# Kernel optimization log

Hardware: AMD Instinct MI355X
Metric: run time of the kernel (lower is better)

## Reference

```python
import jax, jax.numpy as jnp
import numpy as np

SCALES = [2, 4, 8, 16]
UNIT = np.array([0.015, 0.015, 0.015], dtype=np.float32)
VNUM = np.array([64, 64, 64], dtype=np.float32)
OFFSET = (-0.5 * UNIT * VNUM).astype(np.float32)  # -0.48 per axis

N = 8192
MS = [16000, 4000, 512, 64]
CS = [32, 64, 128, 256]


def setup_inputs() -> dict:
    key = jax.random.key(0)
    ks = jax.random.split(key, 1 + 2 * 4)
    extent = (UNIT * VNUM).astype(np.float32)  # 0.96 per axis
    points = (jax.random.uniform(ks[0], (N, 3), dtype=jnp.float32) - 0.5) * extent
    inp = {"points": points, "batch_ids": jnp.zeros((N,), dtype=jnp.int32)}
    for i, (m, c, s) in enumerate(zip(MS, CS, SCALES)):
        grid = 64 // s
        idx = jax.random.randint(ks[1 + 2 * i], (m, 4), 0, grid, dtype=jnp.int32)
        idx = idx.at[:, 0].set(0)  # single batch
        inp[f"indices{i + 1}"] = idx
        inp[f"feats{i + 1}"] = jax.random.normal(ks[2 + 2 * i], (m, c), dtype=jnp.float32)
    return inp


def _three_nn_interpolate(t_xyz, q_xyz, q_feats):
    # t_xyz: [N,3] targets, q_xyz: [M,3] voxel centers, q_feats: [M,C]
    d2 = jnp.sum((t_xyz[:, None, :] - q_xyz[None, :, :]) ** 2, axis=-1)  # [N,M] squared dists
    neg_d, idx = jax.lax.top_k(-d2, 3)  # 3 nearest neighbors
    dist = -neg_d  # squared distances, as returned by pointnet2 three_nn
    dist_recip = 1.0 / (dist + 1e-8)
    weight = dist_recip / jnp.sum(dist_recip, axis=-1, keepdims=True)  # [N,3]
    return jnp.einsum('nk,nkc->nc', weight, q_feats[idx])  # gather + weighted sum


def reference(points, batch_ids, feats1, indices1, feats2, indices2,
              feats3, indices3, feats4, indices4):
    # batch_ids are all zero (single batch); the CUDA kernel restricts the
    # neighbor search to matching batch, so an xyz-only distance is faithful.
    feat_lists = [feats1, feats2, feats3, feats4]
    idx_lists = [indices1, indices2, indices3, indices4]
    outs = []
    for i, s in enumerate(SCALES):
        voxel_extent = (UNIT * s).astype(np.float32)
        # tensor2points: voxel index -> metric center coordinate
        q_xyz = idx_lists[i][:, 1:].astype(jnp.float32) * voxel_extent + OFFSET + 0.5 * voxel_extent
        outs.append(_three_nn_interpolate(points, q_xyz, feat_lists[i]))
    return jnp.concatenate(outs, axis=1)  # [N, 32+64+128+256]
```

## Files before the change

kernel.cpp:

```cpp
#include <hip/hip_runtime.h>

#define INF_F 3.402823466e+38f

struct Params {
  const float* points;
  const int* idx[4];
  const float* feats[4];
  float2* hdr;
  int* counts;
  int2* cellHdr;
  int* fillcur;
  int* mfill;
  int* cellList;
  int* perm;
  int* cursor;
  float* outp;
  int N, totM, totC;
  int M[4], C[4], Mbase[4], colOff[4], G[4], cellBase[4];
  int cellsTot, lenCounts, allocBlocks;
  float ve[4], hv[4], inv_ve[4];
  float off;
};

__device__ __forceinline__ int spread3(int v) {
  return (v & 1) | ((v & 2) << 2) | ((v & 4) << 4) | ((v & 8) << 6);
}
__device__ __forceinline__ int point_bucket(const float* pts, int i) {
  float x = pts[i * 3 + 0], y = pts[i * 3 + 1], z = pts[i * 3 + 2];
  float sc = 16.0f / 0.96f;
  int cx = (int)((x + 0.48f) * sc);
  int cy = (int)((y + 0.48f) * sc);
  int cz = (int)((z + 0.48f) * sc);
  cx = cx < 0 ? 0 : (cx > 15 ? 15 : cx);
  cy = cy < 0 ? 0 : (cy > 15 ? 15 : cy);
  cz = cz < 0 ? 0 : (cz > 15 ? 15 : cz);
  return spread3(cx) | (spread3(cy) << 1) | (spread3(cz) << 2);
}

__device__ __forceinline__ bool lexlt(float da, int ia, float db, int ib) {
  return da < db || (da == db && ia < ib);
}

__global__ __launch_bounds__(256) void zero_kernel(Params pr) {
  int t = blockIdx.x * 256 + threadIdx.x;
  if (t < pr.lenCounts) pr.counts[t] = 0;
  if (t == 0) pr.cursor[0] = 0;
}

__global__ __launch_bounds__(256) void count_kernel(Params pr) {
  int t = blockIdx.x * 256 + threadIdx.x;
  if (t < pr.totM) {
    int s = (t >= pr.Mbase[1]) + (t >= pr.Mbase[2]) + (t >= pr.Mbase[3]);
    int m = t - pr.Mbase[s];
    const int* id = pr.idx[s] + (size_t)m * 4;
    int G = pr.G[s];
    int cell = (id[1] * G + id[2]) * G + id[3];
    atomicAdd(&pr.counts[pr.cellBase[s] + cell], 1);
  } else if (t < pr.totM + pr.N) {
    int i = t - pr.totM;
    atomicAdd(&pr.counts[pr.cellsTot + point_bucket(pr.points, i)], 1);
  }
}

__global__ __launch_bounds__(256) void alloc_kernel(Params pr) {
  int tid = threadIdx.x;
  int lane = tid & 63, wv = tid >> 6;
  if ((int)blockIdx.x < pr.allocBlocks) {
    int c = blockIdx.x * 256 + tid;
    int cnt = (c < pr.cellsTot) ? pr.counts[c] : 0;
    int inc = cnt;
    for (int off = 1; off < 64; off <<= 1) {
      int u = __shfl_up(inc, off);
      if (lane >= off) inc += u;
    }
    int wtotal = __shfl(inc, 63);
    int basev = 0;
    if (lane == 63 && wtotal > 0) basev = atomicAdd(pr.cursor, wtotal);
    basev = __shfl(basev, 63);
    if (c < pr.cellsTot) {
      int st = basev + inc - cnt;
      pr.cellHdr[c] = make_int2(st, cnt);
      pr.fillcur[c] = st;
    }
    return;
  }
  __shared__ int wt[4];
  const int base = pr.cellsTot;
  int v[16]; int sum = 0;
#pragma unroll
  for (int k = 0; k < 16; ++k) { v[k] = pr.counts[base + tid * 16 + k]; sum += v[k]; }
  int inc = sum;
  for (int off = 1; off < 64; off <<= 1) {
    int u = __shfl_up(inc, off);
    if (lane >= off) inc += u;
  }
  if (lane == 63) wt[wv] = inc;
  __syncthreads();
  int wbase = 0;
  for (int w = 0; w < 4; ++w) wbase += (w < wv) ? wt[w] : 0;
  int run = wbase + inc - sum;
#pragma unroll
  for (int k = 0; k < 16; ++k) { pr.mfill[tid * 16 + k] = run; run += v[k]; }
}

__global__ __launch_bounds__(256) void fill_kernel(Params pr) {
  int t = blockIdx.x * 256 + threadIdx.x;
  if (t < pr.totM) {
    int s = (t >= pr.Mbase[1]) + (t >= pr.Mbase[2]) + (t >= pr.Mbase[3]);
    int m = t - pr.Mbase[s];
    const int* id = pr.idx[s] + (size_t)m * 4;
    int G = pr.G[s];
    int cell = (id[1] * G + id[2]) * G + id[3];
    int pos = atomicAdd(&pr.fillcur[pr.cellBase[s] + cell], 1);
    pr.cellList[pos] = m;
  } else if (t < pr.totM + pr.N) {
    int i = t - pr.totM;
    int pos = atomicAdd(&pr.mfill[point_bucket(pr.points, i)], 1);
    pr.perm[pos] = i;
  }
}

__global__ __launch_bounds__(256) void search_kernel(Params pr) {
#pragma clang fp contract(off)
  int wave = blockIdx.x * 4 + (threadIdx.x >> 6);
  if (wave >= 4 * pr.N) return;
  int lane = threadIdx.x & 63;
  int s = wave / pr.N;
  int slot = wave - s * pr.N;
  int pid = pr.perm[slot];
  float px = pr.points[pid * 3 + 0];
  float py = pr.points[pid * 3 + 1];
  float pz = pr.points[pid * 3 + 2];
  int G = pr.G[s];
  float ve = pr.ve[s], hv = pr.hv[s], off = pr.off, inv = pr.inv_ve[s];
  int cx = (int)((px - off) * inv); cx = cx < 0 ? 0 : (cx > G - 1 ? G - 1 : cx);
  int cy = (int)((py - off) * inv); cy = cy < 0 ? 0 : (cy > G - 1 ? G - 1 : cy);
  int cz = (int)((pz - off) * inv); cz = cz < 0 ? 0 : (cz > G - 1 ? G - 1 : cz);
  const int2* hdrc = pr.cellHdr + pr.cellBase[s];
  const int* clist = pr.cellList;

  float bd0 = INF_F, bd1 = INF_F, bd2 = INF_F;
  int bi0 = 0, bi1 = 0, bi2 = 0;

  auto visit_cell = [&](int gx, int gy, int gz) {
    int2 hc = hdrc[(gx * G + gy) * G + gz];
    if (hc.y == 0) return;
    float qx = ((float)gx * ve + off) + hv;
    float qy = ((float)gy * ve + off) + hv;
    float qz = ((float)gz * ve + off) + hv;
    float dxv = px - qx, dyv = py - qy, dzv = pz - qz;
    float dx2 = dxv * dxv;
    float dxy2 = fmaf(dyv, dyv, dx2);
    float d = fmaf(dzv, dzv, dxy2);
    int b = hc.x + hc.y;
    for (int e = hc.x; e < b; ++e) {
      int m = clist[e];
      if (lexlt(d, m, bd2, bi2)) {
        bool l1 = lexlt(d, m, bd1, bi1), l0 = lexlt(d, m, bd0, bi0);
        bd2 = l1 ? bd1 : d;  bi2 = l1 ? bi1 : m;
        bd1 = l0 ? bd0 : (l1 ? d : bd1);
        bi1 = l0 ? bi0 : (l1 ? m : bi1);
        bd0 = l0 ? d : bd0;  bi0 = l0 ? m : bi0;
      }
    }
  };

#pragma unroll
  for (int it = 0; it < 2; ++it) {
    int u = lane + it * 64;
    if (u < 125) {
      int ox = u / 25;
      int rem = u - ox * 25;
      int oy = rem / 5;
      int oz = rem - oy * 5;
      int gx = cx + ox - 2, gy = cy + oy - 2, gz = cz + oz - 2;
      if (gx >= 0 && gx <= G - 1 && gy >= 0 && gy <= G - 1 &&
          gz >= 0 && gz <= G - 1)
        visit_cell(gx, gy, gz);
    }
  }

  bool covered = (cx - 2 <= 0 && cy - 2 <= 0 && cz - 2 <= 0 &&
                  cx + 2 >= G - 1 && cy + 2 >= G - 1 && cz + 2 >= G - 1);
  bool stop = covered;
  if (!stop) {
    float bound = (2.0f + 0.499f) * ve;
    float b2 = bound * bound;
    unsigned long long m0 = __ballot(bd0 < b2);
    unsigned long long m1 = __ballot(bd1 < b2);
    unsigned long long m2 = __ballot(bd2 < b2);
    stop = (__popcll(m0) + __popcll(m1) + __popcll(m2)) >= 3;
  }

  if (!stop) {
    for (int r = 3; r <= 2 * G; ++r) {
      int box = 2 * r + 1;
      int nbox = box * box * box;
      for (int u = lane; u < nbox; u += 64) {
        int ox = u / (box * box);
        int rem = u - ox * (box * box);
        int oy = rem / box;
        int oz = rem - oy * box;
        ox -= r; oy -= r; oz -= r;
        int ax = ox < 0 ? -ox : ox, ay = oy < 0 ? -oy : oy, az = oz < 0 ? -oz : oz;
        int ad = ax > ay ? ax : ay; ad = ad > az ? ad : az;
        if (ad != r) continue;
        int gx = cx + ox, gy = cy + oy, gz = cz + oz;
        if (gx < 0 || gx > G - 1 || gy < 0 || gy > G - 1 || gz < 0 || gz > G - 1)
          continue;
        visit_cell(gx, gy, gz);
      }
      int x0 = cx - r, x1 = cx + r, y0 = cy - r, y1 = cy + r, z0 = cz - r, z1 = cz + r;
      bool cov = (x0 <= 0 && y0 <= 0 && z0 <= 0 &&
                  x1 >= G - 1 && y1 >= G - 1 && z1 >= G - 1);
      if (cov) break;
      float bound = ((float)r + 0.499f) * ve;
      float b2 = bound * bound;
      unsigned long long m0 = __ballot(bd0 < b2);
      unsigned long long m1 = __ballot(bd1 < b2);
      unsigned long long m2 = __ballot(bd2 < b2);
      if ((__popcll(m0) + __popcll(m1) + __popcll(m2)) >= 3) break;
    }
  }

  float md0 = bd0, md1 = bd1, md2 = bd2;
  int mi0 = bi0, mi1 = bi1, mi2 = bi2;
#pragma unroll
  for (int o = 1; o < 64; o <<= 1) {
    float od0 = __shfl_xor(md0, o), od1 = __shfl_xor(md1, o), od2 = __shfl_xor(md2, o);
    int oi0 = __shfl_xor(mi0, o), oi1 = __shfl_xor(mi1, o), oi2 = __shfl_xor(mi2, o);
    bool bw = lexlt(od0, oi0, md0, mi0);
    float xd0 = bw ? od0 : md0, xd1 = bw ? od1 : md1, xd2 = bw ? od2 : md2;
    int   xi0 = bw ? oi0 : mi0, xi1 = bw ? oi1 : mi1, xi2 = bw ? oi2 : mi2;
    float yd0 = bw ? md0 : od0, yd1 = bw ? md1 : od1;
    int   yi0 = bw ? mi0 : oi0, yi1 = bw ? mi1 : oi1;
    bool x1w = lexlt(xd1, xi1, yd0, yi0);
    bool a2 = lexlt(xd2, xi2, yd0, yi0);
    bool c2 = lexlt(xd1, xi1, yd1, yi1);
    md0 = xd0; mi0 = xi0;
    md1 = x1w ? xd1 : yd0;  mi1 = x1w ? xi1 : yi0;
    md2 = x1w ? (a2 ? xd2 : yd0) : (c2 ? xd1 : yd1);
    mi2 = x1w ? (a2 ? xi2 : yi0) : (c2 ? xi1 : yi1);
  }

  if (lane == 0) {
    float r0 = 1.0f / (md0 + 1e-8f);
    float r1 = 1.0f / (md1 + 1e-8f);
    float r2 = 1.0f / (md2 + 1e-8f);
    float sum = (r0 + r1) + r2;
    float2* h = pr.hdr + ((size_t)slot * 4 + s) * 3;
    h[0] = make_float2(r0 / sum, __int_as_float(mi0));
    h[1] = make_float2(r1 / sum, __int_as_float(mi1));
    h[2] = make_float2(r2 / sum, __int_as_float(mi2));
  }
}

__global__ __launch_bounds__(128) void gather_kernel(Params pr) {
#pragma clang fp contract(off)
  int slot = blockIdx.x;
  int pid = pr.perm[slot];
  const float2* h = pr.hdr + (size_t)slot * 12;
  int nC4 = pr.totC >> 2;
  for (int c4 = threadIdx.x; c4 < nC4; c4 += 128) {
    int c = c4 << 2;
    int gs = (c >= pr.colOff[1]) + (c >= pr.colOff[2]) + (c >= pr.colOff[3]);
    int cc = c - pr.colOff[gs];
    float2 h0 = h[gs * 3 + 0], h1 = h[gs * 3 + 1], h2 = h[gs * 3 + 2];
    const float* F = pr.feats[gs];
    int C = pr.C[gs];
    const float4 a  = *(const float4*)(F + (size_t)__float_as_int(h0.y) * C + cc);
    const float4 bq = *(const float4*)(F + (size_t)__float_as_int(h1.y) * C + cc);
    const float4 cq = *(const float4*)(F + (size_t)__float_as_int(h2.y) * C + cc);
    float4 v;
    v.x = (h0.x * a.x + h1.x * bq.x) + h2.x * cq.x;
    v.y = (h0.x * a.y + h1.x * bq.y) + h2.x * cq.y;
    v.z = (h0.x * a.z + h1.x * bq.z) + h2.x * cq.z;
    v.w = (h0.x * a.w + h1.x * bq.w) + h2.x * cq.w;
    *(float4*)(pr.outp + (size_t)pid * pr.totC + c) = v;
  }
}

extern "C" void kernel_launch(void* const* d_in, const int* in_sizes, int n_in,
                              void* d_out, int out_size, void* d_ws, size_t ws_size,
                              hipStream_t stream) {
  (void)n_in; (void)out_size; (void)ws_size;
  Params pr;
  pr.points = (const float*)d_in[0];
  pr.N = in_sizes[0] / 3;
  static const int SC[4] = {2, 4, 8, 16};
  int totM = 0, totC = 0, cellsTot = 0;
  for (int s = 0; s < 4; ++s) {
    pr.idx[s] = (const int*)d_in[2 + 2 * s];
    pr.feats[s] = (const float*)d_in[3 + 2 * s];
    pr.M[s] = in_sizes[2 + 2 * s] / 4;
    pr.C[s] = in_sizes[3 + 2 * s] / pr.M[s];
    pr.Mbase[s] = totM;
    pr.colOff[s] = totC;
    totM += pr.M[s];
    totC += pr.C[s];
    int G = 64 / SC[s];
    pr.G[s] = G;
    pr.cellBase[s] = cellsTot;
    cellsTot += G * G * G;
    float ve = 0.015f * (float)SC[s];
    pr.ve[s] = ve;
    pr.hv[s] = 0.5f * ve;
    pr.inv_ve[s] = 1.0f / ve;
  }
  pr.off = (-0.5f * 0.015f) * 64.0f;
  pr.totM = totM;
  pr.totC = totC;
  pr.cellsTot = cellsTot;
  pr.lenCounts = cellsTot + 4096;
  pr.allocBlocks = (cellsTot + 255) / 256;

  char* ws = (char*)d_ws;
  size_t o = 0;
  pr.hdr = (float2*)(ws + o);     o += (size_t)pr.N * 12 * 8;
  pr.counts = (int*)(ws + o);     o += (size_t)pr.lenCounts * 4;
  pr.cellHdr = (int2*)(ws + o);   o += (size_t)cellsTot * 8;
  pr.fillcur = (int*)(ws + o);    o += (size_t)cellsTot * 4;
  pr.mfill = (int*)(ws + o);      o += (size_t)4096 * 4;
  pr.cellList = (int*)(ws + o);   o += (size_t)totM * 4;
  pr.perm = (int*)(ws + o);       o += (size_t)pr.N * 4;
  pr.cursor = (int*)(ws + o);     o += 64;
  pr.outp = (float*)d_out;

  int cntThreads = totM + pr.N;
  hipLaunchKernelGGL(zero_kernel, dim3((pr.lenCounts + 255) / 256), dim3(256), 0, stream, pr);
  hipLaunchKernelGGL(count_kernel, dim3((cntThreads + 255) / 256), dim3(256), 0, stream, pr);
  hipLaunchKernelGGL(alloc_kernel, dim3(pr.allocBlocks + 1), dim3(256), 0, stream, pr);
  hipLaunchKernelGGL(fill_kernel, dim3((cntThreads + 255) / 256), dim3(256), 0, stream, pr);
  hipLaunchKernelGGL(search_kernel, dim3(pr.N), dim3(256), 0, stream, pr);
  hipLaunchKernelGGL(gather_kernel, dim3(pr.N), dim3(128), 0, stream, pr);
}
```

Before: 130.4 us.

## Fuse search and gather kernels, drop point sorting, inline first two cell entries

Merges the neighbor search and feature gather into one kernel where each block handles one point, with the four waves each searching one scale and passing weights and indices through shared memory. This removes the global header round-trip and one launch. It also drops the Morton-order point permutation and its counting and fill passes. Cell headers grow to int4 so the first two voxel ids are stored inline, saving a cellList load for sparse cells. Losing the spatial sort may reduce cache locality in the search, and the larger headers add load bandwidth.

```diff
diff --git a/kernel.cpp b/kernel.cpp
--- a/kernel.cpp
+++ b/kernel.cpp
@@ -6,145 +6,113 @@
   const float* points;
   const int* idx[4];
   const float* feats[4];
-  float2* hdr;
   int* counts;
-  int2* cellHdr;
+  int4* cellHdr;
   int* fillcur;
-  int* mfill;
   int* cellList;
-  int* perm;
   int* cursor;
   float* outp;
   int N, totM, totC;
   int M[4], C[4], Mbase[4], colOff[4], G[4], cellBase[4];
-  int cellsTot, lenCounts, allocBlocks;
+  int cellsTot, allocBlocks;
   float ve[4], hv[4], inv_ve[4];
   float off;
 };
 
-__device__ __forceinline__ int spread3(int v) {
-  return (v & 1) | ((v & 2) << 2) | ((v & 4) << 4) | ((v & 8) << 6);
-}
-__device__ __forceinline__ int point_bucket(const float* pts, int i) {
-  float x = pts[i * 3 + 0], y = pts[i * 3 + 1], z = pts[i * 3 + 2];
-  float sc = 16.0f / 0.96f;
-  int cx = (int)((x + 0.48f) * sc);
-  int cy = (int)((y + 0.48f) * sc);
-  int cz = (int)((z + 0.48f) * sc);
-  cx = cx < 0 ? 0 : (cx > 15 ? 15 : cx);
-  cy = cy < 0 ? 0 : (cy > 15 ? 15 : cy);
-  cz = cz < 0 ? 0 : (cz > 15 ? 15 : cz);
-  return spread3(cx) | (spread3(cy) << 1) | (spread3(cz) << 2);
-}
-
 __device__ __forceinline__ bool lexlt(float da, int ia, float db, int ib) {
   return da < db || (da == db && ia < ib);
 }
 
 __global__ __launch_bounds__(256) void zero_kernel(Params pr) {
   int t = blockIdx.x * 256 + threadIdx.x;
-  if (t < pr.lenCounts) pr.counts[t] = 0;
+  if (t < pr.cellsTot) pr.counts[t] = 0;
   if (t == 0) pr.cursor[0] = 0;
 }
 
 __global__ __launch_bounds__(256) void count_kernel(Params pr) {
   int t = blockIdx.x * 256 + threadIdx.x;
-  if (t < pr.totM) {
-    int s = (t >= pr.Mbase[1]) + (t >= pr.Mbase[2]) + (t >= pr.Mbase[3]);
-    int m = t - pr.Mbase[s];
-    const int* id = pr.idx[s] + (size_t)m * 4;
-    int G = pr.G[s];
-    int cell = (id[1] * G + id[2]) * G + id[3];
-    atomicAdd(&pr.counts[pr.cellBase[s] + cell], 1);
-  } else if (t < pr.totM + pr.N) {
-    int i = t - pr.totM;
-    atomicAdd(&pr.counts[pr.cellsTot + point_bucket(pr.points, i)], 1);
-  }
+  if (t >= pr.totM) return;
+  int s = (t >= pr.Mbase[1]) + (t >= pr.Mbase[2]) + (t >= pr.Mbase[3]);
+  int m = t - pr.Mbase[s];
+  const int* id = pr.idx[s] + (size_t)m * 4;
+  int G = pr.G[s];
+  int cell = (id[1] * G + id[2]) * G + id[3];
+  atomicAdd(&pr.counts[pr.cellBase[s] + cell], 1);
 }
 
 __global__ __launch_bounds__(256) void alloc_kernel(Params pr) {
   int tid = threadIdx.x;
-  int lane = tid & 63, wv = tid >> 6;
-  if ((int)blockIdx.x < pr.allocBlocks) {
-    int c = blockIdx.x * 256 + tid;
-    int cnt = (c < pr.cellsTot) ? pr.counts[c] : 0;
-    int inc = cnt;
-    for (int off = 1; off < 64; off <<= 1) {
-      int u = __shfl_up(inc, off);
-      if (lane >= off) inc += u;
-    }
-    int wtotal = __shfl(inc, 63);
-    int basev = 0;
-    if (lane == 63 && wtotal > 0) basev = atomicAdd(pr.cursor, wtotal);
-    basev = __shfl(basev, 63);
-    if (c < pr.cellsTot) {
-      int st = basev + inc - cnt;
-      pr.cellHdr[c] = make_int2(st, cnt);
-      pr.fillcur[c] = st;
-    }
-    return;
-  }
-  __shared__ int wt[4];
-  const int base = pr.cellsTot;
-  int v[16]; int sum = 0;
-#pragma unroll
-  for (int k = 0; k < 16; ++k) { v[k] = pr.counts[base + tid * 16 + k]; sum += v[k]; }
-  int inc = sum;
+  int lane = tid & 63;
+  int c = blockIdx.x * 256 + tid;
+  int cnt = (c < pr.cellsTot) ? pr.counts[c] : 0;
+  int inc = cnt;
   for (int off = 1; off < 64; off <<= 1) {
     int u = __shfl_up(inc, off);
     if (lane >= off) inc += u;
   }
-  if (lane == 63) wt[wv] = inc;
-  __syncthreads();
-  int wbase = 0;
-  for (int w = 0; w < 4; ++w) wbase += (w < wv) ? wt[w] : 0;
-  int run = wbase + inc - sum;
-#pragma unroll
-  for (int k = 0; k < 16; ++k) { pr.mfill[tid * 16 + k] = run; run += v[k]; }
+  int wtotal = __shfl(inc, 63);
+  int basev = 0;
+  if (lane == 63 && wtotal > 0) basev = atomicAdd(pr.cursor, wtotal);
+  basev = __shfl(basev, 63);
+  if (c < pr.cellsTot) {
+    int st = basev + inc - cnt;
+    pr.cellHdr[c] = make_int4(st, cnt, 0, 0);
+    pr.fillcur[c] = st;
+  }
 }
 
 __global__ __launch_bounds__(256) void fill_kernel(Params pr) {
   int t = blockIdx.x * 256 + threadIdx.x;
-  if (t < pr.totM) {
-    int s = (t >= pr.Mbase[1]) + (t >= pr.Mbase[2]) + (t >= pr.Mbase[3]);
-    int m = t - pr.Mbase[s];
-    const int* id = pr.idx[s] + (size_t)m * 4;
-    int G = pr.G[s];
-    int cell = (id[1] * G + id[2]) * G + id[3];
-    int pos = atomicAdd(&pr.fillcur[pr.cellBase[s] + cell], 1);
-    pr.cellList[pos] = m;
-  } else if (t < pr.totM + pr.N) {
-    int i = t - pr.totM;
-    int pos = atomicAdd(&pr.mfill[point_bucket(pr.points, i)], 1);
-    pr.perm[pos] = i;
-  }
-}
-
-__global__ __launch_bounds__(256) void search_kernel(Params pr) {
+  if (t >= pr.totM) return;
+  int s = (t >= pr.Mbase[1]) + (t >= pr.Mbase[2]) + (t >= pr.Mbase[3]);
+  int m = t - pr.Mbase[s];
+  const int* id = pr.idx[s] + (size_t)m * 4;
+  int G = pr.G[s];
+  int c = pr.cellBase[s] + (id[1] * G + id[2]) * G + id[3];
+  int pos = atomicAdd(&pr.fillcur[c], 1);
+  pr.cellList[pos] = m;
+  int rel = pos - pr.cellHdr[c].x;
+  if (rel == 0) ((int*)&pr.cellHdr[c])[2] = m;
+  else if (rel == 1) ((int*)&pr.cellHdr[c])[3] = m;
+}
+
+__global__ __launch_bounds__(256) void searchgather_kernel(Params pr) {
 #pragma clang fp contract(off)
-  int wave = blockIdx.x * 4 + (threadIdx.x >> 6);
-  if (wave >= 4 * pr.N) return;
-  int lane = threadIdx.x & 63;
-  int s = wave / pr.N;
-  int slot = wave - s * pr.N;
-  int pid = pr.perm[slot];
-  float px = pr.points[pid * 3 + 0];
-  float py = pr.points[pid * 3 + 1];
-  float pz = pr.points[pid * 3 + 2];
+  __shared__ float wsh[4][3];
+  __shared__ int ish[4][3];
+  int slot = blockIdx.x;
+  int tid = threadIdx.x;
+  int lane = tid & 63;
+  int s = tid >> 6;
+
+  float px = pr.points[slot * 3 + 0];
+  float py = pr.points[slot * 3 + 1];
+  float pz = pr.points[slot * 3 + 2];
   int G = pr.G[s];
   float ve = pr.ve[s], hv = pr.hv[s], off = pr.off, inv = pr.inv_ve[s];
   int cx = (int)((px - off) * inv); cx = cx < 0 ? 0 : (cx > G - 1 ? G - 1 : cx);
   int cy = (int)((py - off) * inv); cy = cy < 0 ? 0 : (cy > G - 1 ? G - 1 : cy);
   int cz = (int)((pz - off) * inv); cz = cz < 0 ? 0 : (cz > G - 1 ? G - 1 : cz);
-  const int2* hdrc = pr.cellHdr + pr.cellBase[s];
+  const int4* hdrc = pr.cellHdr + pr.cellBase[s];
   const int* clist = pr.cellList;
 
   float bd0 = INF_F, bd1 = INF_F, bd2 = INF_F;
   int bi0 = 0, bi1 = 0, bi2 = 0;
 
+  auto consider = [&](float d, int m) {
+    if (lexlt(d, m, bd2, bi2)) {
+      bool l1 = lexlt(d, m, bd1, bi1), l0 = lexlt(d, m, bd0, bi0);
+      bd2 = l1 ? bd1 : d;  bi2 = l1 ? bi1 : m;
+      bd1 = l0 ? bd0 : (l1 ? d : bd1);
+      bi1 = l0 ? bi0 : (l1 ? m : bi1);
+      bd0 = l0 ? d : bd0;  bi0 = l0 ? m : bi0;
+    }
+  };
+
   auto visit_cell = [&](int gx, int gy, int gz) {
-    int2 hc = hdrc[(gx * G + gy) * G + gz];
-    if (hc.y == 0) return;
+    int4 hc = hdrc[(gx * G + gy) * G + gz];
+    int cnt = hc.y;
+    if (cnt == 0) return;
     float qx = ((float)gx * ve + off) + hv;
     float qy = ((float)gy * ve + off) + hv;
     float qz = ((float)gz * ve + off) + hv;
@@ -152,16 +120,11 @@
     float dx2 = dxv * dxv;
     float dxy2 = fmaf(dyv, dyv, dx2);
     float d = fmaf(dzv, dzv, dxy2);
-    int b = hc.x + hc.y;
-    for (int e = hc.x; e < b; ++e) {
-      int m = clist[e];
-      if (lexlt(d, m, bd2, bi2)) {
-        bool l1 = lexlt(d, m, bd1, bi1), l0 = lexlt(d, m, bd0, bi0);
-        bd2 = l1 ? bd1 : d;  bi2 = l1 ? bi1 : m;
-        bd1 = l0 ? bd0 : (l1 ? d : bd1);
-        bi1 = l0 ? bi0 : (l1 ? m : bi1);
-        bd0 = l0 ? d : bd0;  bi0 = l0 ? m : bi0;
-      }
+    consider(d, hc.z);
+    if (cnt > 1) consider(d, hc.w);
+    if (cnt > 2) {
+      int b = hc.x + cnt;
+      for (int e = hc.x + 2; e < b; ++e) consider(d, clist[e]);
     }
   };
 
@@ -248,35 +211,29 @@
     float r1 = 1.0f / (md1 + 1e-8f);
     float r2 = 1.0f / (md2 + 1e-8f);
     float sum = (r0 + r1) + r2;
-    float2* h = pr.hdr + ((size_t)slot * 4 + s) * 3;
-    h[0] = make_float2(r0 / sum, __int_as_float(mi0));
-    h[1] = make_float2(r1 / sum, __int_as_float(mi1));
-    h[2] = make_float2(r2 / sum, __int_as_float(mi2));
-  }
-}
-
-__global__ __launch_bounds__(128) void gather_kernel(Params pr) {
-#pragma clang fp contract(off)
-  int slot = blockIdx.x;
-  int pid = pr.perm[slot];
-  const float2* h = pr.hdr + (size_t)slot * 12;
+    wsh[s][0] = r0 / sum; wsh[s][1] = r1 / sum; wsh[s][2] = r2 / sum;
+    ish[s][0] = mi0; ish[s][1] = mi1; ish[s][2] = mi2;
+  }
+  __syncthreads();
+
   int nC4 = pr.totC >> 2;
-  for (int c4 = threadIdx.x; c4 < nC4; c4 += 128) {
-    int c = c4 << 2;
+  if (tid < nC4) {
+    int c = tid << 2;
     int gs = (c >= pr.colOff[1]) + (c >= pr.colOff[2]) + (c >= pr.colOff[3]);
     int cc = c - pr.colOff[gs];
-    float2 h0 = h[gs * 3 + 0], h1 = h[gs * 3 + 1], h2 = h[gs * 3 + 2];
+    float w0 = wsh[gs][0], w1 = wsh[gs][1], w2 = wsh[gs][2];
+    int g0 = ish[gs][0], g1 = ish[gs][1], g2 = ish[gs][2];
     const float* F = pr.feats[gs];
     int C = pr.C[gs];
-    const float4 a  = *(const float4*)(F + (size_t)__float_as_int(h0.y) * C + cc);
-    const float4 bq = *(const float4*)(F + (size_t)__float_as_int(h1.y) * C + cc);
-    const float4 cq = *(const float4*)(F + (size_t)__float_as_int(h2.y) * C + cc);
+    const float4 a  = *(const float4*)(F + (size_t)g0 * C + cc);
+    const float4 bq = *(const float4*)(F + (size_t)g1 * C + cc);
+    const float4 cq = *(const float4*)(F + (size_t)g2 * C + cc);
     float4 v;
-    v.x = (h0.x * a.x + h1.x * bq.x) + h2.x * cq.x;
-    v.y = (h0.x * a.y + h1.x * bq.y) + h2.x * cq.y;
-    v.z = (h0.x * a.z + h1.x * bq.z) + h2.x * cq.z;
-    v.w = (h0.x * a.w + h1.x * bq.w) + h2.x * cq.w;
-    *(float4*)(pr.outp + (size_t)pid * pr.totC + c) = v;
+    v.x = (w0 * a.x + w1 * bq.x) + w2 * cq.x;
+    v.y = (w0 * a.y + w1 * bq.y) + w2 * cq.y;
+    v.z = (w0 * a.z + w1 * bq.z) + w2 * cq.z;
+    v.w = (w0 * a.w + w1 * bq.w) + w2 * cq.w;
+    *(float4*)(pr.outp + (size_t)slot * pr.totC + c) = v;
   }
 }
 
@@ -311,26 +268,20 @@
   pr.totM = totM;
   pr.totC = totC;
   pr.cellsTot = cellsTot;
-  pr.lenCounts = cellsTot + 4096;
   pr.allocBlocks = (cellsTot + 255) / 256;
 
   char* ws = (char*)d_ws;
   size_t o = 0;
-  pr.hdr = (float2*)(ws + o);     o += (size_t)pr.N * 12 * 8;
-  pr.counts = (int*)(ws + o);     o += (size_t)pr.lenCounts * 4;
-  pr.cellHdr = (int2*)(ws + o);   o += (size_t)cellsTot * 8;
+  pr.cellHdr = (int4*)(ws + o);   o += (size_t)cellsTot * 16;
+  pr.counts = (int*)(ws + o);     o += (size_t)cellsTot * 4;
   pr.fillcur = (int*)(ws + o);    o += (size_t)cellsTot * 4;
-  pr.mfill = (int*)(ws + o);      o += (size_t)4096 * 4;
   pr.cellList = (int*)(ws + o);   o += (size_t)totM * 4;
-  pr.perm = (int*)(ws + o);       o += (size_t)pr.N * 4;
   pr.cursor = (int*)(ws + o);     o += 64;
   pr.outp = (float*)d_out;
 
-  int cntThreads = totM + pr.N;
-  hipLaunchKernelGGL(zero_kernel, dim3((pr.lenCounts + 255) / 256), dim3(256), 0, stream, pr);
-  hipLaunchKernelGGL(count_kernel, dim3((cntThreads + 255) / 256), dim3(256), 0, stream, pr);
-  hipLaunchKernelGGL(alloc_kernel, dim3(pr.allocBlocks + 1), dim3(256), 0, stream, pr);
-  hipLaunchKernelGGL(fill_kernel, dim3((cntThreads + 255) / 256), dim3(256), 0, stream, pr);
-  hipLaunchKernelGGL(search_kernel, dim3(pr.N), dim3(256), 0, stream, pr);
-  hipLaunchKernelGGL(gather_kernel, dim3(pr.N), dim3(128), 0, stream, pr);
-}
+  hipLaunchKernelGGL(zero_kernel, dim3((cellsTot + 255) / 256), dim3(256), 0, stream, pr);
+  hipLaunchKernelGGL(count_kernel, dim3((totM + 255) / 256), dim3(256), 0, stream, pr);
+  hipLaunchKernelGGL(alloc_kernel, dim3(pr.allocBlocks), dim3(256), 0, stream, pr);
+  hipLaunchKernelGGL(fill_kernel, dim3((totM + 255) / 256), dim3(256), 0, stream, pr);
+  hipLaunchKernelGGL(searchgather_kernel, dim3(pr.N), dim3(256), 0, stream, pr);
+}
```

Result: faster. 123.3 us (-5.5%).
